# Optimization experiments

Hardware: AMD Instinct MI355X
Metric: run time of the kernel (lower is better)

## Reference

```python
import jax, jax.numpy as jnp
import numpy as np

BITS = 4
MAXQ = 15          # (1 << BITS) - 1
PACK = 32 // BITS  # 8 values packed per int32


def dequantize(qweight, qzeros, scales, g_idx):
    """GPTQ 4-bit dequant. qweight: [K//8, N] int32, qzeros: [G, N//8] int32,
    scales: [G, N] float, g_idx: [K] int32 -> dense W [K, N] float."""
    N = qweight.shape[1]
    shifts = (jnp.arange(PACK, dtype=jnp.uint32) * BITS)  # [8]
    qw = qweight.astype(jnp.uint32)
    # unpack along K: k = row*8 + j  (matches shifter = (k % 8) * bits)
    w_int = ((qw[:, None, :] >> shifts[None, :, None]) & MAXQ).reshape(-1, N)  # [K, N]
    qz = qzeros.astype(jnp.uint32)
    # unpack along N: n = col*8 + j  (matches zeros_shifter = (n % 8) * bits)
    z_int = ((qz[:, :, None] >> shifts[None, None, :]) & MAXQ).reshape(qzeros.shape[0], -1) + 1  # [G, N]
    dt = scales.dtype
    # group-wise dequant: w = (q - zero) * scale, gathered per-row via g_idx
    return (w_int.astype(dt) - z_int[g_idx].astype(dt)) * scales[g_idx]


def setup_inputs() -> dict:
    key = jax.random.key(0)
    k1, k2, k3, k4, k5 = jax.random.split(key, 5)
    M, K, N, GS = 128, 4096, 11008, 128
    G = K // GS
    x = jax.random.normal(k1, (M, K), dtype=jnp.float32)
    qweight = jax.random.randint(k2, (K // PACK, N), 0, 2147483647, dtype=jnp.int32)
    qzeros = jax.random.randint(k3, (G, N // PACK), 0, 2147483647, dtype=jnp.int32)
    scales = jax.random.uniform(k4, (G, N), dtype=jnp.float32, minval=0.001, maxval=0.01)
    bias = jax.random.normal(k5, (N,), dtype=jnp.float32)
    g_idx = (jnp.arange(K, dtype=jnp.int32) // GS).astype(jnp.int32)
    return {"x": x, "qweight": qweight, "qzeros": qzeros, "scales": scales,
            "bias": bias, "g_idx": g_idx}


def reference(x, qweight, qzeros, scales, bias, g_idx):
    w = dequantize(qweight, qzeros, scales, g_idx)  # [K, N]
    return x @ w + bias
```

## Files before the change

### kernel.cpp

```cpp
#include <hip/hip_runtime.h>
#include <stdint.h>


#define M_DIM 128
#define K_DIM 4096
#define N_DIM 11008
#define GS    128
#define NG    32
#define SPLIT 4
#define GPB   (NG / SPLIT)
#define NB    (N_DIM / 64)
#define PART_ELEMS ((size_t)NB * 4 * 2048)

typedef _Float16 half8  __attribute__((ext_vector_type(8)));
typedef _Float16 half2t __attribute__((ext_vector_type(2)));
typedef _Float16 half4t __attribute__((ext_vector_type(4)));
typedef float    f32x4  __attribute__((ext_vector_type(4)));

__global__ void k_prep(const float* __restrict__ x, const int* __restrict__ qzeros,
                       const float* __restrict__ scales,
                       _Float16* __restrict__ xh, _Float16* __restrict__ szp) {
    int b = blockIdx.x, tid = threadIdx.x;
    if (b < 512) {
        int i = (b * 256 + tid) * 4;
        float4 v = *(const float4*)(x + i);
        half4t o;
        o[0] = (_Float16)v.x; o[1] = (_Float16)v.y;
        o[2] = (_Float16)v.z; o[3] = (_Float16)v.w;
        *(half4t*)(xh + i) = o;
    } else {
        b -= 512;
        int g = b / 43;
        int n = (b - g * 43) * 256 + tid;
        unsigned qz = (unsigned)qzeros[g * (N_DIM / 8) + (n >> 3)];
        float s  = scales[g * N_DIM + n];
        float z1 = (float)((qz >> ((n & 7) * 4)) & 15u) + 1.0f;
        half4t o;
        o[0] = (_Float16)s;
        o[1] = (_Float16)(s * 0.0625f);
        o[2] = (_Float16)(-(z1 * s));
        o[3] = o[2];
        *(half4t*)(szp + (size_t)(g * N_DIM + n) * 4) = o;
    }
}

__device__ __forceinline__ void load_lds16(const void* g, void* l) {
    __builtin_amdgcn_global_load_lds(
        (const __attribute__((address_space(1))) unsigned int*)g,
        (__attribute__((address_space(3))) unsigned int*)l, 16, 0, 0);
}

__device__ __forceinline__ half8 dequant8(unsigned q, half2t S2, half2t Z2) {
    const half2t BIAS = __builtin_bit_cast(half2t, 0x64006400u);
    half2t w[4];
#pragma unroll
    for (int p = 0; p < 4; ++p) {
        unsigned r = __builtin_amdgcn_perm(q, q, 0x00010001u * (unsigned)p);
        unsigned t = (r & 0x00F0000Fu) | 0x64006400u;
        w[p] = __builtin_elementwise_fma(__builtin_bit_cast(half2t, t) - BIAS, S2, Z2);
    }
    half4t lo = __builtin_shufflevector(w[0], w[1], 0, 1, 2, 3);
    half4t hi = __builtin_shufflevector(w[2], w[3], 0, 1, 2, 3);
    return __builtin_shufflevector(lo, hi, 0, 1, 2, 3, 4, 5, 6, 7);
}

__global__ __launch_bounds__(512, 4)
void k_gemm(const _Float16* __restrict__ xh,
            const int*      __restrict__ qweight,
            const _Float16* __restrict__ szp,
            _Float16*       __restrict__ part)
{
    __shared__ _Float16 As[2][128 * 128];

    const int tid  = threadIdx.x;
    const int lane = tid & 63;
    const int w    = tid >> 6;
    const int wx   = w & 1;
    const int wy   = (w >> 1) & 1;
    const int kh   = w >> 2;
    const int q    = lane >> 4;
    const int lr   = lane & 15;

    const int n0 = blockIdx.x * 64;
    const int g0 = blockIdx.y * GPB;
    int ncol[2] = { n0 + wx * 32 + lr, n0 + wx * 32 + lr + 16 };

    f32x4 acc[4][2];
#pragma unroll
    for (int f = 0; f < 4; ++f)
#pragma unroll
        for (int h = 0; h < 2; ++h)
            acc[f][h] = (f32x4){0.f, 0.f, 0.f, 0.f};

    int cm[4], ckb[4];
#pragma unroll
    for (int it = 0; it < 4; ++it) {
        int c = it * 512 + tid;
        cm[it]  = c >> 4;
        ckb[it] = (c & 15) ^ (cm[it] & 15);
    }
    const int wave_lds = w * 64 * 8;

#pragma unroll
    for (int it = 0; it < 4; ++it)
        load_lds16(xh + (size_t)cm[it] * K_DIM + g0 * GS + ckb[it] * 8,
                   &As[0][it * 512 * 8 + wave_lds]);
    unsigned qwn[4];
    half4t   szn[2];
#pragma unroll
    for (int t = 0; t < 2; ++t)
#pragma unroll
        for (int h = 0; h < 2; ++h)
            qwn[t * 2 + h] = (unsigned)qweight[(size_t)(g0 * 16 + (kh * 2 + t) * 4 + q) * N_DIM + ncol[h]];
#pragma unroll
    for (int h = 0; h < 2; ++h)
        szn[h] = *(const half4t*)(szp + ((size_t)g0 * N_DIM + ncol[h]) * 4);

    int p = 0;
    for (int g = 0; g < GPB; ++g) {
        unsigned qw[4];
        half4t   sz[2];
#pragma unroll
        for (int i = 0; i < 4; ++i) qw[i] = qwn[i];
#pragma unroll
        for (int h = 0; h < 2; ++h) sz[h] = szn[h];

        __syncthreads();

        if (g + 1 < GPB) {
            int gn = g0 + g + 1;
#pragma unroll
            for (int it = 0; it < 4; ++it)
                load_lds16(xh + (size_t)cm[it] * K_DIM + gn * GS + ckb[it] * 8,
                           &As[p ^ 1][it * 512 * 8 + wave_lds]);
#pragma unroll
            for (int t = 0; t < 2; ++t)
#pragma unroll
                for (int h = 0; h < 2; ++h)
                    qwn[t * 2 + h] = (unsigned)qweight[(size_t)(gn * 16 + (kh * 2 + t) * 4 + q) * N_DIM + ncol[h]];
#pragma unroll
            for (int h = 0; h < 2; ++h)
                szn[h] = *(const half4t*)(szp + ((size_t)gn * N_DIM + ncol[h]) * 4);
        }

        half2t S2[2], Z2[2];
#pragma unroll
        for (int h = 0; h < 2; ++h) {
            S2[h] = __builtin_shufflevector(sz[h], sz[h], 0, 1);
            Z2[h] = __builtin_shufflevector(sz[h], sz[h], 2, 3);
        }

#pragma unroll
        for (int t = 0; t < 2; ++t) {
            const int kk = kh * 2 + t;
            half8 bf[2];
#pragma unroll
            for (int h = 0; h < 2; ++h)
                bf[h] = dequant8(qw[t * 2 + h], S2[h], Z2[h]);
#pragma unroll
            for (int f = 0; f < 4; ++f) {
                int m   = wy * 64 + f * 16 + lr;
                int kb2 = (kk * 4 + q) ^ lr;
                half8 af = *(const half8*)(&As[p][m * 128 + kb2 * 8]);
#pragma unroll
                for (int h = 0; h < 2; ++h)
                    acc[f][h] = __builtin_amdgcn_mfma_f32_16x16x32_f16(af, bf[h], acc[f][h], 0, 0, 0);
            }
        }
        p ^= 1;
    }

    __syncthreads();
    float* red = (float*)&As[0][0];
    const int pid = w & 3;
    if (w >= 4) {
#pragma unroll
        for (int f = 0; f < 4; ++f)
#pragma unroll
            for (int h = 0; h < 2; ++h)
                *(f32x4*)(red + pid * 2048 + (f * 2 + h) * 256 + lane * 4) = acc[f][h];
    }
    __syncthreads();
    if (w < 4) {
        _Float16* ph = part + (size_t)blockIdx.y * PART_ELEMS
                     + (size_t)(blockIdx.x * 4 + pid) * 2048;
#pragma unroll
        for (int f = 0; f < 4; ++f) {
#pragma unroll
            for (int h = 0; h < 2; ++h) {
                f32x4 o = acc[f][h] + *(const f32x4*)(red + pid * 2048 + (f * 2 + h) * 256 + lane * 4);
                half4t ov;
#pragma unroll
                for (int r = 0; r < 4; ++r) ov[r] = (_Float16)o[r];
                *(half4t*)(ph + ((f * 2 + h) * 64 + lane) * 4) = ov;
            }
        }
    }
}

__global__ void k_reduce(const _Float16* __restrict__ part, const float* __restrict__ bias,
                         float* __restrict__ out) {
    int t = blockIdx.x * 256 + threadIdx.x;
    int lane = t & 63, fh = (t >> 6) & 7, pid = (t >> 9) & 3, nb = t >> 11;
    int f = fh >> 1, h = fh & 1, wy = pid >> 1, wx = pid & 1;
    int q = lane >> 4, lr = lane & 15;
    int m0 = wy * 64 + f * 16 + q * 4;
    int n  = nb * 64 + wx * 32 + h * 16 + lr;
    f32x4 sv = (f32x4){0.f, 0.f, 0.f, 0.f};
#pragma unroll
    for (int s = 0; s < SPLIT; ++s) {
        half4t v = *(const half4t*)(part + s * PART_ELEMS + (size_t)t * 4);
#pragma unroll
        for (int r = 0; r < 4; ++r) sv[r] += (float)v[r];
    }
    float b = bias[n];
#pragma unroll
    for (int r = 0; r < 4; ++r)
        out[(size_t)(m0 + r) * N_DIM + n] = sv[r] + b;
}

extern "C" void kernel_launch(void* const* d_in, const int* in_sizes, int n_in,
                              void* d_out, int out_size, void* d_ws, size_t ws_size,
                              hipStream_t stream) {
    const float* x       = (const float*)d_in[0];
    const int*   qweight = (const int*)d_in[1];
    const int*   qzeros  = (const int*)d_in[2];
    const float* scales  = (const float*)d_in[3];
    const float* bias    = (const float*)d_in[4];

    char* ws = (char*)d_ws;
    _Float16* xh   = (_Float16*)ws;
    _Float16* szp  = (_Float16*)(ws + 1048576);
    _Float16* part = (_Float16*)(ws + 1048576 + 2818048);

    k_prep  <<<dim3(1888),         dim3(256), 0, stream>>>(x, qzeros, scales, xh, szp);
    k_gemm  <<<dim3(NB, SPLIT),    dim3(512), 0, stream>>>(xh, qweight, szp, part);
    k_reduce<<<dim3(1376),         dim3(256), 0, stream>>>(part, bias, (float*)d_out);
}
```

Before: 105.0 us.

## Replace split-K partial buffer and reduce kernel with atomic adds into bias-initialized output

The prep kernel now also fills the output with the broadcast bias, and the GEMM kernel accumulates its split-K partial sums directly into the output with float atomic adds. This removes the fp16 partial buffer and the separate reduce kernel launch. The scale/zero table is also packed to two halves per column, with the scaled 1/16 term rebuilt in registers. In exchange it adds atomic traffic (four-way contention per output element) and makes the summation order nondeterministic.

```diff
diff --git a/kernel.cpp b/kernel.cpp
--- a/kernel.cpp
+++ b/kernel.cpp
@@ -10,7 +10,6 @@
 #define SPLIT 4
 #define GPB   (NG / SPLIT)
 #define NB    (N_DIM / 64)
-#define PART_ELEMS ((size_t)NB * 4 * 2048)
 
 typedef _Float16 half8  __attribute__((ext_vector_type(8)));
 typedef _Float16 half2t __attribute__((ext_vector_type(2)));
@@ -18,8 +17,9 @@
 typedef float    f32x4  __attribute__((ext_vector_type(4)));
 
 __global__ void k_prep(const float* __restrict__ x, const int* __restrict__ qzeros,
-                       const float* __restrict__ scales,
-                       _Float16* __restrict__ xh, _Float16* __restrict__ szp) {
+                       const float* __restrict__ scales, const float* __restrict__ bias,
+                       _Float16* __restrict__ xh, _Float16* __restrict__ szp,
+                       float* __restrict__ out) {
     int b = blockIdx.x, tid = threadIdx.x;
     if (b < 512) {
         int i = (b * 256 + tid) * 4;
@@ -28,19 +28,22 @@
         o[0] = (_Float16)v.x; o[1] = (_Float16)v.y;
         o[2] = (_Float16)v.z; o[3] = (_Float16)v.w;
         *(half4t*)(xh + i) = o;
-    } else {
+    } else if (b < 1888) {
         b -= 512;
         int g = b / 43;
         int n = (b - g * 43) * 256 + tid;
         unsigned qz = (unsigned)qzeros[g * (N_DIM / 8) + (n >> 3)];
         float s  = scales[g * N_DIM + n];
         float z1 = (float)((qz >> ((n & 7) * 4)) & 15u) + 1.0f;
-        half4t o;
+        half2t o;
         o[0] = (_Float16)s;
-        o[1] = (_Float16)(s * 0.0625f);
-        o[2] = (_Float16)(-(z1 * s));
-        o[3] = o[2];
-        *(half4t*)(szp + (size_t)(g * N_DIM + n) * 4) = o;
+        o[1] = (_Float16)(-(z1 * s));
+        *(half2t*)(szp + (size_t)(g * N_DIM + n) * 2) = o;
+    } else {
+        int i = ((b - 1888) * 256 + tid) * 4;
+        int m = i / N_DIM;
+        int n = i - m * N_DIM;
+        *(float4*)(out + i) = *(const float4*)(bias + n);
     }
 }
 
@@ -68,7 +71,7 @@
 void k_gemm(const _Float16* __restrict__ xh,
             const int*      __restrict__ qweight,
             const _Float16* __restrict__ szp,
-            _Float16*       __restrict__ part)
+            float*          __restrict__ out)
 {
     __shared__ _Float16 As[2][128 * 128];
 
@@ -106,7 +109,7 @@
         load_lds16(xh + (size_t)cm[it] * K_DIM + g0 * GS + ckb[it] * 8,
                    &As[0][it * 512 * 8 + wave_lds]);
     unsigned qwn[4];
-    half4t   szn[2];
+    half2t   szn[2];
 #pragma unroll
     for (int t = 0; t < 2; ++t)
 #pragma unroll
@@ -114,12 +117,12 @@
             qwn[t * 2 + h] = (unsigned)qweight[(size_t)(g0 * 16 + (kh * 2 + t) * 4 + q) * N_DIM + ncol[h]];
 #pragma unroll
     for (int h = 0; h < 2; ++h)
-        szn[h] = *(const half4t*)(szp + ((size_t)g0 * N_DIM + ncol[h]) * 4);
+        szn[h] = *(const half2t*)(szp + ((size_t)g0 * N_DIM + ncol[h]) * 2);
 
     int p = 0;
     for (int g = 0; g < GPB; ++g) {
         unsigned qw[4];
-        half4t   sz[2];
+        half2t   sz[2];
 #pragma unroll
         for (int i = 0; i < 4; ++i) qw[i] = qwn[i];
 #pragma unroll
@@ -140,14 +143,16 @@
                     qwn[t * 2 + h] = (unsigned)qweight[(size_t)(gn * 16 + (kh * 2 + t) * 4 + q) * N_DIM + ncol[h]];
 #pragma unroll
             for (int h = 0; h < 2; ++h)
-                szn[h] = *(const half4t*)(szp + ((size_t)gn * N_DIM + ncol[h]) * 4);
+                szn[h] = *(const half2t*)(szp + ((size_t)gn * N_DIM + ncol[h]) * 2);
         }
 
         half2t S2[2], Z2[2];
 #pragma unroll
         for (int h = 0; h < 2; ++h) {
-            S2[h] = __builtin_shufflevector(sz[h], sz[h], 0, 1);
-            Z2[h] = __builtin_shufflevector(sz[h], sz[h], 2, 3);
+            S2[h][0] = sz[h][0];
+            S2[h][1] = sz[h][0] * (_Float16)0.0625f;
+            Z2[h][0] = sz[h][1];
+            Z2[h][1] = sz[h][1];
         }
 
 #pragma unroll
@@ -182,41 +187,18 @@
     }
     __syncthreads();
     if (w < 4) {
-        _Float16* ph = part + (size_t)blockIdx.y * PART_ELEMS
-                     + (size_t)(blockIdx.x * 4 + pid) * 2048;
 #pragma unroll
         for (int f = 0; f < 4; ++f) {
+            int mrow = wy * 64 + f * 16 + q * 4;
 #pragma unroll
             for (int h = 0; h < 2; ++h) {
                 f32x4 o = acc[f][h] + *(const f32x4*)(red + pid * 2048 + (f * 2 + h) * 256 + lane * 4);
-                half4t ov;
-#pragma unroll
-                for (int r = 0; r < 4; ++r) ov[r] = (_Float16)o[r];
-                *(half4t*)(ph + ((f * 2 + h) * 64 + lane) * 4) = ov;
+#pragma unroll
+                for (int r = 0; r < 4; ++r)
+                    unsafeAtomicAdd(&out[(size_t)(mrow + r) * N_DIM + ncol[h]], o[r]);
             }
         }
     }
-}
-
-__global__ void k_reduce(const _Float16* __restrict__ part, const float* __restrict__ bias,
-                         float* __restrict__ out) {
-    int t = blockIdx.x * 256 + threadIdx.x;
-    int lane = t & 63, fh = (t >> 6) & 7, pid = (t >> 9) & 3, nb = t >> 11;
-    int f = fh >> 1, h = fh & 1, wy = pid >> 1, wx = pid & 1;
-    int q = lane >> 4, lr = lane & 15;
-    int m0 = wy * 64 + f * 16 + q * 4;
-    int n  = nb * 64 + wx * 32 + h * 16 + lr;
-    f32x4 sv = (f32x4){0.f, 0.f, 0.f, 0.f};
-#pragma unroll
-    for (int s = 0; s < SPLIT; ++s) {
-        half4t v = *(const half4t*)(part + s * PART_ELEMS + (size_t)t * 4);
-#pragma unroll
-        for (int r = 0; r < 4; ++r) sv[r] += (float)v[r];
-    }
-    float b = bias[n];
-#pragma unroll
-    for (int r = 0; r < 4; ++r)
-        out[(size_t)(m0 + r) * N_DIM + n] = sv[r] + b;
 }
 
 extern "C" void kernel_launch(void* const* d_in, const int* in_sizes, int n_in,
@@ -229,11 +211,10 @@
     const float* bias    = (const float*)d_in[4];
 
     char* ws = (char*)d_ws;
-    _Float16* xh   = (_Float16*)ws;
-    _Float16* szp  = (_Float16*)(ws + 1048576);
-    _Float16* part = (_Float16*)(ws + 1048576 + 2818048);
-
-    k_prep  <<<dim3(1888),         dim3(256), 0, stream>>>(x, qzeros, scales, xh, szp);
-    k_gemm  <<<dim3(NB, SPLIT),    dim3(512), 0, stream>>>(xh, qweight, szp, part);
-    k_reduce<<<dim3(1376),         dim3(256), 0, stream>>>(part, bias, (float*)d_out);
-}
+    _Float16* xh  = (_Float16*)ws;
+    _Float16* szp = (_Float16*)(ws + 1048576);
+
+    k_prep<<<dim3(3264),       dim3(256), 0, stream>>>(x, qzeros, scales, bias,
+                                                       xh, szp, (float*)d_out);
+    k_gemm<<<dim3(NB, SPLIT),  dim3(512), 0, stream>>>(xh, qweight, szp, (float*)d_out);
+}
```

Result: slower. 110.8 us (+5.6%).

## Give each wave full M with 16 N columns and pack scale/zero as half2

Applied to the files above, without the earlier changes.

The wave tiling changes from a 2x2 split of M and N to each wave covering all 128 rows and a single 16-column N strip. Each weight element is then dequantized once per block, not once per M-half, which removes duplicated dequant ALU work and duplicated qweight loads. In exchange, each wave reads twice as many A fragments from LDS per MFMA. The prep kernel now stores scale and negative zero·scale as half2 instead of half4, halving that buffer, and the scale/16 term is computed in the loop.

```diff
diff --git a/kernel.cpp b/kernel.cpp
--- a/kernel.cpp
+++ b/kernel.cpp
@@ -35,12 +35,10 @@
         unsigned qz = (unsigned)qzeros[g * (N_DIM / 8) + (n >> 3)];
         float s  = scales[g * N_DIM + n];
         float z1 = (float)((qz >> ((n & 7) * 4)) & 15u) + 1.0f;
-        half4t o;
+        half2t o;
         o[0] = (_Float16)s;
-        o[1] = (_Float16)(s * 0.0625f);
-        o[2] = (_Float16)(-(z1 * s));
-        o[3] = o[2];
-        *(half4t*)(szp + (size_t)(g * N_DIM + n) * 4) = o;
+        o[1] = (_Float16)(-(z1 * s));
+        *(half2t*)(szp + (size_t)(g * N_DIM + n) * 2) = o;
     }
 }
 
@@ -75,22 +73,19 @@
     const int tid  = threadIdx.x;
     const int lane = tid & 63;
     const int w    = tid >> 6;
-    const int wx   = w & 1;
-    const int wy   = (w >> 1) & 1;
+    const int ns   = w & 3;
     const int kh   = w >> 2;
     const int q    = lane >> 4;
     const int lr   = lane & 15;
 
     const int n0 = blockIdx.x * 64;
     const int g0 = blockIdx.y * GPB;
-    int ncol[2] = { n0 + wx * 32 + lr, n0 + wx * 32 + lr + 16 };
-
-    f32x4 acc[4][2];
-#pragma unroll
-    for (int f = 0; f < 4; ++f)
-#pragma unroll
-        for (int h = 0; h < 2; ++h)
-            acc[f][h] = (f32x4){0.f, 0.f, 0.f, 0.f};
+    const int ncol = n0 + ns * 16 + lr;
+
+    f32x4 acc[8];
+#pragma unroll
+    for (int f = 0; f < 8; ++f)
+        acc[f] = (f32x4){0.f, 0.f, 0.f, 0.f};
 
     int cm[4], ckb[4];
 #pragma unroll
@@ -105,25 +100,20 @@
     for (int it = 0; it < 4; ++it)
         load_lds16(xh + (size_t)cm[it] * K_DIM + g0 * GS + ckb[it] * 8,
                    &As[0][it * 512 * 8 + wave_lds]);
-    unsigned qwn[4];
-    half4t   szn[2];
+    unsigned qwn[2];
+    half2t   szn;
 #pragma unroll
     for (int t = 0; t < 2; ++t)
-#pragma unroll
-        for (int h = 0; h < 2; ++h)
-            qwn[t * 2 + h] = (unsigned)qweight[(size_t)(g0 * 16 + (kh * 2 + t) * 4 + q) * N_DIM + ncol[h]];
-#pragma unroll
-    for (int h = 0; h < 2; ++h)
-        szn[h] = *(const half4t*)(szp + ((size_t)g0 * N_DIM + ncol[h]) * 4);
+        qwn[t] = (unsigned)qweight[(size_t)(g0 * 16 + (kh * 2 + t) * 4 + q) * N_DIM + ncol];
+    szn = *(const half2t*)(szp + ((size_t)g0 * N_DIM + ncol) * 2);
 
     int p = 0;
     for (int g = 0; g < GPB; ++g) {
-        unsigned qw[4];
-        half4t   sz[2];
-#pragma unroll
-        for (int i = 0; i < 4; ++i) qw[i] = qwn[i];
-#pragma unroll
-        for (int h = 0; h < 2; ++h) sz[h] = szn[h];
+        unsigned qw[2];
+        half2t   sz;
+#pragma unroll
+        for (int i = 0; i < 2; ++i) qw[i] = qwn[i];
+        sz = szn;
 
         __syncthreads();
 
@@ -135,36 +125,26 @@
                            &As[p ^ 1][it * 512 * 8 + wave_lds]);
 #pragma unroll
             for (int t = 0; t < 2; ++t)
-#pragma unroll
-                for (int h = 0; h < 2; ++h)
-                    qwn[t * 2 + h] = (unsigned)qweight[(size_t)(gn * 16 + (kh * 2 + t) * 4 + q) * N_DIM + ncol[h]];
-#pragma unroll
-            for (int h = 0; h < 2; ++h)
-                szn[h] = *(const half4t*)(szp + ((size_t)gn * N_DIM + ncol[h]) * 4);
+                qwn[t] = (unsigned)qweight[(size_t)(gn * 16 + (kh * 2 + t) * 4 + q) * N_DIM + ncol];
+            szn = *(const half2t*)(szp + ((size_t)gn * N_DIM + ncol) * 2);
         }
 
-        half2t S2[2], Z2[2];
-#pragma unroll
-        for (int h = 0; h < 2; ++h) {
-            S2[h] = __builtin_shufflevector(sz[h], sz[h], 0, 1);
-            Z2[h] = __builtin_shufflevector(sz[h], sz[h], 2, 3);
-        }
+        half2t S2, Z2;
+        S2[0] = sz[0];
+        S2[1] = sz[0] * (_Float16)0.0625f;
+        Z2[0] = sz[1];
+        Z2[1] = sz[1];
 
 #pragma unroll
         for (int t = 0; t < 2; ++t) {
             const int kk = kh * 2 + t;
-            half8 bf[2];
-#pragma unroll
-            for (int h = 0; h < 2; ++h)
-                bf[h] = dequant8(qw[t * 2 + h], S2[h], Z2[h]);
-#pragma unroll
-            for (int f = 0; f < 4; ++f) {
-                int m   = wy * 64 + f * 16 + lr;
-                int kb2 = (kk * 4 + q) ^ lr;
+            half8 bf = dequant8(qw[t], S2, Z2);
+            const int kb2 = (kk * 4 + q) ^ lr;
+#pragma unroll
+            for (int f = 0; f < 8; ++f) {
+                int m = f * 16 + lr;
                 half8 af = *(const half8*)(&As[p][m * 128 + kb2 * 8]);
-#pragma unroll
-                for (int h = 0; h < 2; ++h)
-                    acc[f][h] = __builtin_amdgcn_mfma_f32_16x16x32_f16(af, bf[h], acc[f][h], 0, 0, 0);
+                acc[f] = __builtin_amdgcn_mfma_f32_16x16x32_f16(af, bf, acc[f], 0, 0, 0);
             }
         }
         p ^= 1;
@@ -172,28 +152,22 @@
 
     __syncthreads();
     float* red = (float*)&As[0][0];
-    const int pid = w & 3;
-    if (w >= 4) {
-#pragma unroll
-        for (int f = 0; f < 4; ++f)
-#pragma unroll
-            for (int h = 0; h < 2; ++h)
-                *(f32x4*)(red + pid * 2048 + (f * 2 + h) * 256 + lane * 4) = acc[f][h];
+    if (kh == 1) {
+#pragma unroll
+        for (int f = 0; f < 8; ++f)
+            *(f32x4*)(red + ns * 2048 + f * 256 + lane * 4) = acc[f];
     }
     __syncthreads();
-    if (w < 4) {
+    if (kh == 0) {
         _Float16* ph = part + (size_t)blockIdx.y * PART_ELEMS
-                     + (size_t)(blockIdx.x * 4 + pid) * 2048;
-#pragma unroll
-        for (int f = 0; f < 4; ++f) {
-#pragma unroll
-            for (int h = 0; h < 2; ++h) {
-                f32x4 o = acc[f][h] + *(const f32x4*)(red + pid * 2048 + (f * 2 + h) * 256 + lane * 4);
-                half4t ov;
-#pragma unroll
-                for (int r = 0; r < 4; ++r) ov[r] = (_Float16)o[r];
-                *(half4t*)(ph + ((f * 2 + h) * 64 + lane) * 4) = ov;
-            }
+                     + (size_t)(blockIdx.x * 4 + ns) * 2048;
+#pragma unroll
+        for (int f = 0; f < 8; ++f) {
+            f32x4 o = acc[f] + *(const f32x4*)(red + ns * 2048 + f * 256 + lane * 4);
+            half4t ov;
+#pragma unroll
+            for (int r = 0; r < 4; ++r) ov[r] = (_Float16)o[r];
+            *(half4t*)(ph + (f * 64 + lane) * 4) = ov;
         }
     }
 }
@@ -201,11 +175,10 @@
 __global__ void k_reduce(const _Float16* __restrict__ part, const float* __restrict__ bias,
                          float* __restrict__ out) {
     int t = blockIdx.x * 256 + threadIdx.x;
-    int lane = t & 63, fh = (t >> 6) & 7, pid = (t >> 9) & 3, nb = t >> 11;
-    int f = fh >> 1, h = fh & 1, wy = pid >> 1, wx = pid & 1;
+    int lane = t & 63, f = (t >> 6) & 7, ns = (t >> 9) & 3, nb = t >> 11;
     int q = lane >> 4, lr = lane & 15;
-    int m0 = wy * 64 + f * 16 + q * 4;
-    int n  = nb * 64 + wx * 32 + h * 16 + lr;
+    int m0 = f * 16 + q * 4;
+    int n  = nb * 64 + ns * 16 + lr;
     f32x4 sv = (f32x4){0.f, 0.f, 0.f, 0.f};
 #pragma unroll
     for (int s = 0; s < SPLIT; ++s) {
@@ -231,7 +204,7 @@
     char* ws = (char*)d_ws;
     _Float16* xh   = (_Float16*)ws;
     _Float16* szp  = (_Float16*)(ws + 1048576);
-    _Float16* part = (_Float16*)(ws + 1048576 + 2818048);
+    _Float16* part = (_Float16*)(ws + 1048576 + 1409024);
 
     k_prep  <<<dim3(1888),         dim3(256), 0, stream>>>(x, qzeros, scales, xh, szp);
     k_gemm  <<<dim3(NB, SPLIT),    dim3(512), 0, stream>>>(xh, qweight, szp, part);
```

Measured after the change: 101.0 us. 3.8% less time.
